# Kernel optimization log

Hardware: AMD Instinct MI355X
Metric: run time of the kernel (lower is better)

The kernel has to match this reference:

```python
import jax, jax.numpy as jnp
import numpy as np


def setup_inputs() -> dict:
    key = jax.random.key(0)
    ks = jax.random.split(key, 16)
    B, S, D = 2, 2048, 1024
    H, SH, RH = 16, 1, 3
    hd = D // H
    w = 1.0 / np.sqrt(D)
    return {
        "x": jax.random.normal(ks[0], (B, S, D), jnp.float32),
        "Wq": jax.random.normal(ks[1], (D, D), jnp.float32) * w,
        "bq": jnp.zeros((D,), jnp.float32),
        "Wk": jax.random.normal(ks[2], (D, D), jnp.float32) * w,
        "bk": jnp.zeros((D,), jnp.float32),
        "Wv": jax.random.normal(ks[3], (D, D), jnp.float32) * w,
        "bv": jnp.zeros((D,), jnp.float32),
        "Wproj": jax.random.normal(ks[4], (D, D), jnp.float32) * w,
        "bproj": jnp.zeros((D,), jnp.float32),
        "Wr": jax.random.normal(ks[5], (D, H - SH), jnp.float32) * w,
        "br": jnp.zeros((H - SH,), jnp.float32),
        "Ws": jax.random.normal(ks[6], (D, 2), jnp.float32) * w,
        "bs": jnp.zeros((2,), jnp.float32),
        "temperature": jnp.zeros((H, 1, 1), jnp.float32),
        "query_embedding": jax.random.truncated_normal(ks[7], -2.0, 2.0, (H, 1, hd), jnp.float32) * 0.02,
        "num_heads": H,
        "shared_heads": SH,
        "routed_heads": RH,
    }


def reference(x, Wq, bq, Wk, bk, Wv, bv, Wproj, bproj, Wr, br, Ws, bs,
              temperature, query_embedding, num_heads, shared_heads, routed_heads):
    B, S, D = x.shape
    H = num_heads
    hd = D // H

    def split_heads(t):  # [B,S,D] -> [B,H,S,hd]
        return t.reshape(B, S, H, hd).transpose(0, 2, 1, 3)

    q = split_heads(x @ Wq + bq)
    k = split_heads(x @ Wk + bk)
    v = split_heads(x @ Wv + bv)

    # L2-normalize q along head_dim, add learned query embedding, scale by softplus(temperature)
    q_norm = q * jax.lax.rsqrt(jnp.sum(q * q, axis=-1, keepdims=True) + 1e-12)
    q_scaled = (q_norm + query_embedding[None]) * jax.nn.softplus(temperature)[None]

    attn = jnp.einsum('bhqd,bhkd->bhqk', q_scaled, k) / jnp.sqrt(jnp.float32(hd))
    attn = jax.nn.softmax(attn, axis=-1)
    o = jnp.einsum('bhqk,bhkd->bhqd', attn, v)
    o = o.transpose(0, 2, 1, 3).reshape(B, S, D)  # [B,S,D]

    # Routed-head gating via top-k router
    gates = jax.nn.softmax(o @ Wr + br, axis=-1)          # [B,S,H-SH]
    _, idx = jax.lax.top_k(gates, routed_heads)           # [B,S,RH]
    mask = jax.nn.one_hot(idx, H - shared_heads, dtype=gates.dtype).sum(axis=2)
    routed_gates = gates * mask * jnp.float32(routed_heads)

    # Shared-head gating
    sw = jax.nn.softmax(o @ Ws + bs, axis=-1)             # [B,S,2]
    shared_gates = sw * jnp.float32(shared_heads)
    w0 = sw * 2.0
    shared_gates = w0[..., 0:1] * shared_gates
    routed_gates = w0[..., 1:2] * routed_gates
    masked_gates = jnp.concatenate([shared_gates, routed_gates], axis=-1)

    # einsum('bnh,bnd->bnd') sums over h: scales o by sum of gates
    o = masked_gates.sum(axis=-1, keepdims=True) * o
    return o @ Wproj + bproj
```

## Files before the change

### kernel.cpp

```cpp
#include <hip/hip_runtime.h>
#include <hip/hip_bf16.h>

typedef unsigned short ushort_t;
typedef unsigned int uint_t;

typedef __attribute__((ext_vector_type(8))) short bf8;
typedef __attribute__((ext_vector_type(4))) float f4;
typedef __attribute__((ext_vector_type(16))) float f16v;

__device__ __forceinline__ float bf2f(ushort_t u) {
    unsigned int x = ((unsigned int)u) << 16;
    return __uint_as_float(x);
}
__device__ __forceinline__ ushort_t f2bf(float f) {
    unsigned int x = __float_as_uint(f);
    unsigned int r = x + 0x7fffu + ((x >> 16) & 1u);
    return (ushort_t)(r >> 16);
}
__device__ __forceinline__ uint_t pack2bf(float a, float b) {
    return (uint_t)f2bf(a) | ((uint_t)f2bf(b) << 16);
}
__device__ __forceinline__ uint_t pack2bf_fast(float a, float b) {
    uint_t au = __float_as_uint(a) + 0x8000u;
    uint_t bu = __float_as_uint(b) + 0x8000u;
    return __builtin_amdgcn_perm(bu, au, 0x07060302);
}
__device__ __forceinline__ float exp2_fast(float x) {
    float r; asm("v_exp_f32 %0, %1" : "=v"(r) : "v"(x)); return r;
}
__device__ __forceinline__ uint_t cvtpk_bf16(float lo, float hi) {
    uint_t r; asm("v_cvt_pk_bf16_f32 %0, %1, %2" : "=v"(r) : "v"(lo), "v"(hi)); return r;
}
__device__ __forceinline__ void pl32swap(uint_t &a, uint_t &b) {
    asm("v_permlane32_swap_b32 %0, %1" : "+v"(a), "+v"(b));
}

__device__ __forceinline__ void gl2lds16(const ushort_t* g, ushort_t* l) {
    __builtin_amdgcn_global_load_lds(
        (const __attribute__((address_space(1))) void*)g,
        (__attribute__((address_space(3))) void*)l, 16, 0, 0);
}

__device__ __forceinline__ void waitl0() {
    asm volatile("s_waitcnt lgkmcnt(0)" ::: "memory");
    __builtin_amdgcn_sched_barrier(0);
}

__global__ __launch_bounds__(256)
void prep(const float* __restrict__ x, ushort_t* __restrict__ xb,
          const float* __restrict__ Wr, const float* __restrict__ Ws,
          ushort_t* __restrict__ Wg,
          const float* __restrict__ W0, const float* __restrict__ W1,
          const float* __restrict__ W2, const float* __restrict__ W3,
          ushort_t* __restrict__ T0, ushort_t* __restrict__ T1,
          ushort_t* __restrict__ T2, ushort_t* __restrict__ T3)
{
    __shared__ float tile[32][33];
    int bid = blockIdx.x;
    int t = threadIdx.x;
    if (bid < 4096) {
        int i = bid * 256 + t;
        float4 v = ((const float4*)x)[i];
        uint2 o;
        o.x = pack2bf(v.x, v.y);
        o.y = pack2bf(v.z, v.w);
        ((uint2*)xb)[i] = o;
    } else if (bid < 4224) {
        int idx = (bid - 4096) * 256 + t;
        int c = idx >> 10, d = idx & 1023;
        float v = 0.f;
        if (c < 15) v = Wr[(size_t)d * 15 + c];
        else if (c < 17) v = Ws[(size_t)d * 2 + (c - 15)];
        Wg[idx] = f2bf(v);
    } else {
        int idx = bid - 4224;
        int z = idx >> 10, r10 = idx & 1023;
        int k0 = (r10 & 31) * 32, n0 = (r10 >> 5) * 32;
        const float* W; ushort_t* T;
        switch (z) {
            case 0: W = W0; T = T0; break;
            case 1: W = W1; T = T1; break;
            case 2: W = W2; T = T2; break;
            default: W = W3; T = T3; break;
        }
        int r = t >> 3, c4 = (t & 7) * 4;
        float4 v = *(const float4*)&W[(size_t)(k0 + r) * 1024 + n0 + c4];
        tile[r][c4 + 0] = v.x; tile[r][c4 + 1] = v.y;
        tile[r][c4 + 2] = v.z; tile[r][c4 + 3] = v.w;
        __syncthreads();
        int n = t >> 3, kk = (t & 7) * 4;
        uint2 o;
        o.x = pack2bf(tile[kk][n], tile[kk + 1][n]);
        o.y = pack2bf(tile[kk + 2][n], tile[kk + 3][n]);
        *(uint2*)&T[(size_t)(n0 + n) * 1024 + k0 + kk] = o;
    }
}

__global__ __launch_bounds__(256)
void gemmQKV(const ushort_t* __restrict__ A, const ushort_t* __restrict__ Wt3,
             const float* __restrict__ bq, const float* __restrict__ bk,
             const float* __restrict__ bv,
             ushort_t* __restrict__ Qb, ushort_t* __restrict__ Kw,
             ushort_t* __restrict__ VTw,
             const float* __restrict__ temp, const float* __restrict__ emb)
{
    const int K = 1024;
    __shared__ ushort_t As[128 * 64];
    __shared__ ushort_t Bs[64 * 64];

    int t = threadIdx.x;
    int m0 = blockIdx.x * 128;
    int y = blockIdx.y;
    int region = y >> 4;
    int n0r = (y & 15) * 64;
    int head = y & 15;

    int lane = t & 63, w = t >> 6;
    int lm = lane & 15, quad = lane >> 4;
    int wm = w * 32;

    f4 acc[8] = {};

    int srow = t >> 3;
    int schunk = ((t & 7) ^ (srow & 7)) * 8;
    const ushort_t* pA = &A[(size_t)(m0 + srow) * K + schunk];
    const ushort_t* pB = &Wt3[(size_t)(y * 64 + srow) * K + schunk];
    const size_t rstep = (size_t)32 * K;

    for (int k0 = 0; k0 < K; k0 += 64) {
        #pragma unroll
        for (int j = 0; j < 4; j++)
            gl2lds16(pA + j * rstep, &As[(t + j * 256) * 8]);
        #pragma unroll
        for (int j = 0; j < 2; j++)
            gl2lds16(pB + j * rstep, &Bs[(t + j * 256) * 8]);
        pA += 64; pB += 64;
        __syncthreads();

        #pragma unroll
        for (int ks = 0; ks < 2; ks++) {
            int rc = ((ks * 4 + quad) ^ (lm & 7)) * 8;
            bf8 af[2], bfr[4];
            #pragma unroll
            for (int mi = 0; mi < 2; mi++)
                af[mi] = *(bf8*)&As[(wm + mi * 16 + lm) * 64 + rc];
            #pragma unroll
            for (int ni = 0; ni < 4; ni++)
                bfr[ni] = *(bf8*)&Bs[(ni * 16 + lm) * 64 + rc];
            if (region == 2) {
                #pragma unroll
                for (int mi = 0; mi < 2; mi++)
                #pragma unroll
                for (int ni = 0; ni < 4; ni++)
                    acc[mi * 4 + ni] = __builtin_amdgcn_mfma_f32_16x16x32_bf16(af[mi], bfr[ni], acc[mi * 4 + ni], 0, 0, 0);
            } else {
                #pragma unroll
                for (int ni = 0; ni < 4; ni++)
                #pragma unroll
                for (int mi = 0; mi < 2; mi++)
                    acc[ni * 2 + mi] = __builtin_amdgcn_mfma_f32_16x16x32_bf16(bfr[ni], af[mi], acc[ni * 2 + mi], 0, 0, 0);
            }
        }
        __syncthreads();
    }

    if (region == 0) {
        float sp = log1pf(__expf(temp[head]));
        float qs = sp * 0.18033688011112042f;
        f4 bv4[4], ev4[4];
        #pragma unroll
        for (int ni = 0; ni < 4; ni++) {
            bv4[ni] = *(const f4*)&bq[n0r + ni * 16 + quad * 4];
            ev4[ni] = *(const f4*)&emb[head * 64 + ni * 16 + quad * 4];
        }
        #pragma unroll
        for (int mi = 0; mi < 2; mi++) {
            float v[4][4];
            float ss = 0.f;
            #pragma unroll
            for (int ni = 0; ni < 4; ni++)
            #pragma unroll
            for (int i = 0; i < 4; i++) {
                v[ni][i] = acc[ni * 2 + mi][i] + bv4[ni][i];
                ss += v[ni][i] * v[ni][i];
            }
            ss += __shfl_xor(ss, 16, 64);
            ss += __shfl_xor(ss, 32, 64);
            float rs = rsqrtf(ss + 1e-12f);
            int tok = m0 + wm + mi * 16 + lm;
            int b = tok >> 11, s = tok & 2047;
            size_t rowb = (((size_t)(b * 16 + head)) * 2048 + s) * 64;
            #pragma unroll
            for (int ni = 0; ni < 4; ni++) {
                uint2 o;
                o.x = pack2bf((v[ni][0] * rs + ev4[ni][0]) * qs,
                              (v[ni][1] * rs + ev4[ni][1]) * qs);
                o.y = pack2bf((v[ni][2] * rs + ev4[ni][2]) * qs,
                              (v[ni][3] * rs + ev4[ni][3]) * qs);
                *(uint2*)&Qb[rowb + ni * 16 + quad * 4] = o;
            }
        }
    } else if (region == 1) {
        f4 bv4[4];
        #pragma unroll
        for (int ni = 0; ni < 4; ni++)
            bv4[ni] = *(const f4*)&bk[n0r + ni * 16 + quad * 4];
        #pragma unroll
        for (int mi = 0; mi < 2; mi++) {
            int tok = m0 + wm + mi * 16 + lm;
            int b = tok >> 11, s = tok & 2047;
            size_t rowb = (((size_t)(b * 16 + head)) * 2048 + s) * 64;
            #pragma unroll
            for (int ni = 0; ni < 4; ni++) {
                uint2 o;
                o.x = pack2bf(acc[ni * 2 + mi][0] + bv4[ni][0], acc[ni * 2 + mi][1] + bv4[ni][1]);
                o.y = pack2bf(acc[ni * 2 + mi][2] + bv4[ni][2], acc[ni * 2 + mi][3] + bv4[ni][3]);
                *(uint2*)&Kw[rowb + ni * 16 + quad * 4] = o;
            }
        }
    } else {
        float bvv[4];
        #pragma unroll
        for (int ni = 0; ni < 4; ni++) bvv[ni] = bv[n0r + ni * 16 + lm];
        #pragma unroll
        for (int mi = 0; mi < 2; mi++) {
            int gr0 = m0 + wm + mi * 16 + quad * 4;
            int b = gr0 >> 11, s0 = gr0 & 2047;
            #pragma unroll
            for (int ni = 0; ni < 4; ni++) {
                int d = ni * 16 + lm;
                uint2 o;
                o.x = pack2bf(acc[mi * 4 + ni][0] + bvv[ni], acc[mi * 4 + ni][1] + bvv[ni]);
                o.y = pack2bf(acc[mi * 4 + ni][2] + bvv[ni], acc[mi * 4 + ni][3] + bvv[ni]);
                *(uint2*)&VTw[(((size_t)(b * 16 + head)) * 64 + d) * 2048 + s0] = o;
            }
        }
    }
}

__global__ __launch_bounds__(256)
void gemmP(const ushort_t* __restrict__ A, const ushort_t* __restrict__ Wt,
           const float* __restrict__ bias, const float* __restrict__ G,
           float* __restrict__ out, int M, int N, int K)
{
    __shared__ ushort_t As[64 * 64];
    __shared__ ushort_t Bs[128 * 64];

    int t = threadIdx.x;
    int m0 = blockIdx.x * 64, n0 = blockIdx.y * 128;
    int lane = t & 63, w = t >> 6;
    int lm = lane & 15, quad = lane >> 4;
    int wm = (w >> 1) * 32, wn = (w & 1) * 64;

    f4 acc[4][2] = {};

    int srow = t >> 3;
    int schunk = ((t & 7) ^ (srow & 7)) * 8;
    const ushort_t* pA = &A[(size_t)(m0 + srow) * K + schunk];
    const ushort_t* pB = &Wt[(size_t)(n0 + srow) * K + schunk];
    const size_t rstep = (size_t)32 * K;

    for (int k0 = 0; k0 < K; k0 += 64) {
        gl2lds16(pA, &As[t * 8]);
        gl2lds16(pA + rstep, &As[(t + 256) * 8]);
        #pragma unroll
        for (int j = 0; j < 4; j++)
            gl2lds16(pB + j * rstep, &Bs[(t + j * 256) * 8]);
        pA += 64; pB += 64;
        __syncthreads();

        #pragma unroll
        for (int ks = 0; ks < 2; ks++) {
            int rc = ((ks * 4 + quad) ^ (lm & 7)) * 8;
            bf8 af[2], bfr[4];
            #pragma unroll
            for (int mi = 0; mi < 2; mi++)
                af[mi] = *(bf8*)&As[(wm + mi * 16 + lm) * 64 + rc];
            #pragma unroll
            for (int ni = 0; ni < 4; ni++)
                bfr[ni] = *(bf8*)&Bs[(wn + ni * 16 + lm) * 64 + rc];
            #pragma unroll
            for (int ni = 0; ni < 4; ni++)
            #pragma unroll
            for (int mi = 0; mi < 2; mi++)
                acc[ni][mi] = __builtin_amdgcn_mfma_f32_16x16x32_bf16(bfr[ni], af[mi], acc[ni][mi], 0, 0, 0);
        }
        __syncthreads();
    }

    f4 bv4[4];
    #pragma unroll
    for (int ni = 0; ni < 4; ni++)
        bv4[ni] = *(const f4*)&bias[n0 + wn + ni * 16 + quad * 4];
    #pragma unroll
    for (int mi = 0; mi < 2; mi++) {
        int tok = m0 + wm + mi * 16 + lm;
        float g = G[tok];
        size_t rowb = (size_t)tok * N + n0 + wn;
        #pragma unroll
        for (int ni = 0; ni < 4; ni++) {
            f4 o;
            #pragma unroll
            for (int i = 0; i < 4; i++) o[i] = g * acc[ni][mi][i] + bv4[ni][i];
            *(f4*)&out[rowb + ni * 16 + quad * 4] = o;
        }
    }
}

__global__ __launch_bounds__(256)
void attn(const ushort_t* __restrict__ Q, const ushort_t* __restrict__ K,
          const ushort_t* __restrict__ VT, ushort_t* __restrict__ Opart,
          float* __restrict__ Lw, int kps)
{
    __shared__ ushort_t Ks[64 * 72];
    __shared__ ushort_t Vt[64 * 72];

    int t = threadIdx.x, lane = t & 63, w = t >> 6;
    int l31 = lane & 31;
    uint_t hi = lane >> 5;
    int bid = blockIdx.x;
    int bh = bid & 31, qt = (bid >> 5) & 15, ks = bid >> 9;
    size_t base = (size_t)bh * 2048 * 64;

    int tok = qt * 128 + w * 32 + l31;
    const ushort_t* qp = &Q[base + (size_t)tok * 64 + hi * 8];
    bf8 qa[4];
    #pragma unroll
    for (int c = 0; c < 4; c++) qa[c] = *(const bf8*)(qp + c * 16);

    float l_part = 0.f;
    f16v o_acc[2] = {};

    int sr = t >> 3, sc = (t & 7) * 8;
    const ushort_t* kp = &K[base + (size_t)(ks * kps + sr) * 64 + sc];
    const ushort_t* vp = &VT[base + (size_t)sr * 2048 + ks * kps + sc];

    uint4 rk0 = *(const uint4*)(kp);
    uint4 rk1 = *(const uint4*)(kp + 32 * 64);
    uint4 rv0 = *(const uint4*)(vp);
    uint4 rv1 = *(const uint4*)(vp + 32 * 2048);
    kp += 64 * 64; vp += 64;

    int iters = kps >> 6;
    for (int it = 0; it < iters; ++it) {
        *(uint4*)&Ks[sr * 72 + sc] = rk0;
        *(uint4*)&Ks[(sr + 32) * 72 + sc] = rk1;
        *(uint4*)&Vt[sr * 72 + sc] = rv0;
        *(uint4*)&Vt[(sr + 32) * 72 + sc] = rv1;
        __syncthreads();

        rk0 = *(const uint4*)(kp);
        rk1 = *(const uint4*)(kp + 32 * 64);
        rv0 = *(const uint4*)(vp);
        rv1 = *(const uint4*)(vp + 32 * 2048);
        kp += 64 * 64; vp += 64;

        bf8 pf[4];
        #pragma unroll
        for (int kt2 = 0; kt2 < 2; kt2++) {
            f16v s = {};
            #pragma unroll
            for (int c = 0; c < 4; c++) {
                bf8 kf = *(bf8*)&Ks[(kt2 * 32 + l31) * 72 + c * 16 + hi * 8];
                s = __builtin_amdgcn_mfma_f32_32x32x16_bf16(kf, qa[c], s, 0, 0, 0);
            }
            uint_t px[4], py[4];
            #pragma unroll
            for (int g = 0; g < 4; g++) {
                float p0 = exp2_fast(s[g * 4 + 0]);
                float p1 = exp2_fast(s[g * 4 + 1]);
                float p2 = exp2_fast(s[g * 4 + 2]);
                float p3 = exp2_fast(s[g * 4 + 3]);
                l_part += (p0 + p1) + (p2 + p3);
                px[g] = cvtpk_bf16(p0, p1);
                py[g] = cvtpk_bf16(p2, p3);
            }
            #pragma unroll
            for (int cc = 0; cc < 2; cc++) {
                uint_t ax = px[2 * cc], bx = px[2 * cc + 1];
                uint_t ay = py[2 * cc], by = py[2 * cc + 1];
                pl32swap(ax, bx);
                pl32swap(ay, by);
                uint4 u;
                u.x = ax; u.y = ay; u.z = bx; u.w = by;
                pf[kt2 * 2 + cc] = *(bf8*)&u;
            }
        }

        #pragma unroll
        for (int c = 0; c < 4; c++) {
            #pragma unroll
            for (int dt = 0; dt < 2; dt++) {
                bf8 vf = *(bf8*)&Vt[(dt * 32 + l31) * 72 + c * 16 + hi * 8];
                o_acc[dt] = __builtin_amdgcn_mfma_f32_32x32x16_bf16(vf, pf[c], o_acc[dt], 0, 0, 0);
            }
        }
        __syncthreads();
    }

    l_part += __shfl_xor(l_part, 32, 64);
    if (hi == 0) Lw[((size_t)ks * 32 + bh) * 2048 + tok] = l_part;

    size_t pbase = (((size_t)(ks * 32 + bh)) * 2048 + tok) * 64;
    #pragma unroll
    for (int dt = 0; dt < 2; dt++)
    #pragma unroll
    for (int g = 0; g < 4; g++) {
        int d0 = dt * 32 + g * 8 + hi * 4;
        uint2 o;
        o.x = pack2bf_fast(o_acc[dt][g * 4 + 0], o_acc[dt][g * 4 + 1]);
        o.y = pack2bf_fast(o_acc[dt][g * 4 + 2], o_acc[dt][g * 4 + 3]);
        *(uint2*)&Opart[pbase + d0] = o;
    }
}

__global__ __launch_bounds__(256)
void fuseCR(const ushort_t* __restrict__ Opart, const float* __restrict__ Lw,
            const ushort_t* __restrict__ Wg, const float* __restrict__ br,
            const float* __restrict__ bs, ushort_t* __restrict__ Ob,
            float* __restrict__ G, int splits)
{
    __shared__ ushort_t Obs[16 * 1032];
    __shared__ float rl_s[16][16];
    __shared__ float Ls[16][21];

    int t = threadIdx.x;
    int tokg0 = blockIdx.x * 16;
    int b = tokg0 >> 11, st0 = tokg0 & 2047;

    {
        int h = t >> 4, tt = t & 15;
        size_t row = (size_t)(b * 16 + h) * 2048 + st0 + tt;
        float l = 0.f;
        #pragma unroll 4
        for (int s = 0; s < splits; s++) l += Lw[(size_t)s * 65536 + row];
        rl_s[h][tt] = 1.f / l;
    }
    __syncthreads();

    {
        int tt = t >> 4, dc = (t & 15) * 4;
        #pragma unroll 4
        for (int h = 0; h < 16; h++) {
            size_t rbase = ((size_t)(b * 16 + h) * 2048 + st0 + tt) * 64 + dc;
            float v0 = 0.f, v1 = 0.f, v2 = 0.f, v3 = 0.f;
            #pragma unroll 4
            for (int s = 0; s < splits; s++) {
                uint2 p = *(const uint2*)&Opart[(size_t)s * 4194304 + rbase];
                v0 += bf2f(p.x & 0xffff);
                v1 += bf2f(p.x >> 16);
                v2 += bf2f(p.y & 0xffff);
                v3 += bf2f(p.y >> 16);
            }
            float rl = rl_s[h][tt];
            v0 *= rl; v1 *= rl; v2 *= rl; v3 *= rl;
            uint2 o;
            o.x = pack2bf(v0, v1);
            o.y = pack2bf(v2, v3);
            *(uint2*)&Obs[tt * 1032 + h * 64 + dc] = o;
            *(uint2*)&Ob[((size_t)(tokg0 + tt)) * 1024 + h * 64 + dc] = o;
        }
    }
    __syncthreads();

    if (t < 64) {
        int lm = t & 15, quad = t >> 4;
        const ushort_t* b0p = &Wg[(size_t)lm * 1024 + quad * 8];
        const ushort_t* b1p = &Wg[(size_t)(16 + lm) * 1024 + quad * 8];
        f4 acc0 = {}, acc1 = {};
        for (int k0 = 0; k0 < 1024; k0 += 32) {
            bf8 a  = *(const bf8*)&Obs[lm * 1032 + k0 + quad * 8];
            bf8 b0 = *(const bf8*)(b0p + k0);
            bf8 b1 = *(const bf8*)(b1p + k0);
            acc0 = __builtin_amdgcn_mfma_f32_16x16x32_bf16(a, b0, acc0, 0, 0, 0);
            acc1 = __builtin_amdgcn_mfma_f32_16x16x32_bf16(a, b1, acc1, 0, 0, 0);
        }
        #pragma unroll
        for (int i = 0; i < 4; i++) {
            int tl = quad * 4 + i;
            Ls[tl][lm] = acc0[i];
            if (lm == 0) Ls[tl][16] = acc1[i];
        }
        waitl0();

        if (t < 16) {
            float v[15];
            float mx = -1e30f;
            #pragma unroll
            for (int c = 0; c < 15; c++) { v[c] = Ls[t][c] + br[c]; mx = fmaxf(mx, v[c]); }
            float sum = 0.f;
            #pragma unroll
            for (int c = 0; c < 15; c++) { v[c] = __expf(v[c] - mx); sum += v[c]; }
            float inv = 1.f / sum;
            float t3 = 0.f;
            for (int r = 0; r < 3; r++) {
                int bi = 0; float bv = -1e30f;
                #pragma unroll
                for (int c = 0; c < 15; c++) if (v[c] > bv) { bv = v[c]; bi = c; }
                t3 += bv; v[bi] = -1e30f;
            }
            t3 *= inv;
            float a0 = Ls[t][15] + bs[0], a1 = Ls[t][16] + bs[1];
            float m2 = fmaxf(a0, a1);
            float e0 = __expf(a0 - m2), e1 = __expf(a1 - m2);
            G[tokg0 + t] = (2.f * e0 + 6.f * e1 * t3) / (e0 + e1);
        }
    }
}

extern "C" void kernel_launch(void* const* d_in, const int* in_sizes, int n_in,
                              void* d_out, int out_size, void* d_ws, size_t ws_size,
                              hipStream_t stream)
{
    const float* x     = (const float*)d_in[0];
    const float* Wq    = (const float*)d_in[1];
    const float* bq    = (const float*)d_in[2];
    const float* Wk    = (const float*)d_in[3];
    const float* bk    = (const float*)d_in[4];
    const float* Wv    = (const float*)d_in[5];
    const float* bv    = (const float*)d_in[6];
    const float* Wproj = (const float*)d_in[7];
    const float* bproj = (const float*)d_in[8];
    const float* Wr    = (const float*)d_in[9];
    const float* br    = (const float*)d_in[10];
    const float* Ws    = (const float*)d_in[11];
    const float* bs    = (const float*)d_in[12];
    const float* temp  = (const float*)d_in[13];
    const float* emb   = (const float*)d_in[14];

    const int M = 4096, N = 1024, Kd = 1024;

    char* ws = (char*)d_ws;
    ushort_t* Kw    = (ushort_t*)ws;
    ushort_t* VTw   = (ushort_t*)(ws + 8388608);
    ushort_t* Qb    = (ushort_t*)(ws + 16777216);
    ushort_t* Wtp   = (ushort_t*)(ws + 25165824);
    float*    Gw    = (float*)(ws + 27262976);
    ushort_t* Wg    = (ushort_t*)(ws + 27279360);
    ushort_t* Wt3   = (ushort_t*)(ws + 27869184);
    ushort_t* Opart = (ushort_t*)(ws + 27869184);
    ushort_t* xb    = (ushort_t*)(ws + 34160640);
    ushort_t* Ob    = Qb;

    int SK;
    float* Lw;
    if (ws_size >= 62472192) {
        SK = 4;
        Lw = (float*)(ws + 61423616);
    } else {
        SK = 2;
        Lw = (float*)(ws + 27344896);
    }

    prep<<<8320, 256, 0, stream>>>(x, xb, Wr, Ws, Wg, Wq, Wk, Wv, Wproj,
        Wt3, Wt3 + 1048576, Wt3 + 2097152, Wtp);

    gemmQKV<<<dim3(32, 48), 256, 0, stream>>>(xb, Wt3, bq, bk, bv,
        Qb, Kw, VTw, temp, emb);

    attn<<<512 * SK, 256, 0, stream>>>(Qb, Kw, VTw, Opart, Lw, 2048 / SK);

    fuseCR<<<256, 256, 0, stream>>>(Opart, Lw, Wg, br, bs, Ob, Gw, SK);

    gemmP<<<dim3(64, 8), 256, 0, stream>>>(Ob, Wtp, bproj, Gw, (float*)d_out, M, N, Kd);
}
```

Before: 237.0 us.

## Double-buffer K/V shared tiles in attention and fix split-K to two

Measured after the change: 235.1 us. About the same (-0.8%).

```diff
diff --git a/kernel.cpp b/kernel.cpp
--- a/kernel.cpp
+++ b/kernel.cpp
@@ -312,8 +312,8 @@
           const ushort_t* __restrict__ VT, ushort_t* __restrict__ Opart,
           float* __restrict__ Lw, int kps)
 {
-    __shared__ ushort_t Ks[64 * 72];
-    __shared__ ushort_t Vt[64 * 72];
+    __shared__ ushort_t Ks[2][64 * 72];
+    __shared__ ushort_t Vt[2][64 * 72];
 
     int t = threadIdx.x, lane = t & 63, w = t >> 6;
     int l31 = lane & 31;
@@ -340,28 +340,44 @@
     uint4 rv0 = *(const uint4*)(vp);
     uint4 rv1 = *(const uint4*)(vp + 32 * 2048);
     kp += 64 * 64; vp += 64;
-
+    *(uint4*)&Ks[0][sr * 72 + sc] = rk0;
+    *(uint4*)&Ks[0][(sr + 32) * 72 + sc] = rk1;
+    *(uint4*)&Vt[0][sr * 72 + sc] = rv0;
+    *(uint4*)&Vt[0][(sr + 32) * 72 + sc] = rv1;
+    rk0 = *(const uint4*)(kp);
+    rk1 = *(const uint4*)(kp + 32 * 64);
+    rv0 = *(const uint4*)(vp);
+    rv1 = *(const uint4*)(vp + 32 * 2048);
+    kp += 64 * 64; vp += 64;
+    __syncthreads();
+
+    int cur = 0;
     int iters = kps >> 6;
     for (int it = 0; it < iters; ++it) {
-        *(uint4*)&Ks[sr * 72 + sc] = rk0;
-        *(uint4*)&Ks[(sr + 32) * 72 + sc] = rk1;
-        *(uint4*)&Vt[sr * 72 + sc] = rv0;
-        *(uint4*)&Vt[(sr + 32) * 72 + sc] = rv1;
-        __syncthreads();
-
+        {
+            ushort_t* Kw_ = &Ks[cur ^ 1][0];
+            ushort_t* Vw_ = &Vt[cur ^ 1][0];
+            *(uint4*)&Kw_[sr * 72 + sc] = rk0;
+            *(uint4*)&Kw_[(sr + 32) * 72 + sc] = rk1;
+            *(uint4*)&Vw_[sr * 72 + sc] = rv0;
+            *(uint4*)&Vw_[(sr + 32) * 72 + sc] = rv1;
+        }
         rk0 = *(const uint4*)(kp);
         rk1 = *(const uint4*)(kp + 32 * 64);
         rv0 = *(const uint4*)(vp);
         rv1 = *(const uint4*)(vp + 32 * 2048);
         kp += 64 * 64; vp += 64;
 
+        const ushort_t* Kr = &Ks[cur][0];
+        const ushort_t* Vr = &Vt[cur][0];
+
         bf8 pf[4];
         #pragma unroll
         for (int kt2 = 0; kt2 < 2; kt2++) {
             f16v s = {};
             #pragma unroll
             for (int c = 0; c < 4; c++) {
-                bf8 kf = *(bf8*)&Ks[(kt2 * 32 + l31) * 72 + c * 16 + hi * 8];
+                bf8 kf = *(bf8*)&Kr[(kt2 * 32 + l31) * 72 + c * 16 + hi * 8];
                 s = __builtin_amdgcn_mfma_f32_32x32x16_bf16(kf, qa[c], s, 0, 0, 0);
             }
             uint_t px[4], py[4];
@@ -391,11 +407,12 @@
         for (int c = 0; c < 4; c++) {
             #pragma unroll
             for (int dt = 0; dt < 2; dt++) {
-                bf8 vf = *(bf8*)&Vt[(dt * 32 + l31) * 72 + c * 16 + hi * 8];
+                bf8 vf = *(bf8*)&Vr[(dt * 32 + l31) * 72 + c * 16 + hi * 8];
                 o_acc[dt] = __builtin_amdgcn_mfma_f32_32x32x16_bf16(vf, pf[c], o_acc[dt], 0, 0, 0);
             }
         }
         __syncthreads();
+        cur ^= 1;
     }
 
     l_part += __shfl_xor(l_part, 32, 64);
@@ -537,20 +554,13 @@
     ushort_t* Wtp   = (ushort_t*)(ws + 25165824);
     float*    Gw    = (float*)(ws + 27262976);
     ushort_t* Wg    = (ushort_t*)(ws + 27279360);
+    float*    Lw    = (float*)(ws + 27344896);
     ushort_t* Wt3   = (ushort_t*)(ws + 27869184);
     ushort_t* Opart = (ushort_t*)(ws + 27869184);
     ushort_t* xb    = (ushort_t*)(ws + 34160640);
     ushort_t* Ob    = Qb;
 
-    int SK;
-    float* Lw;
-    if (ws_size >= 62472192) {
-        SK = 4;
-        Lw = (float*)(ws + 61423616);
-    } else {
-        SK = 2;
-        Lw = (float*)(ws + 27344896);
-    }
+    const int SK = 2;
 
     prep<<<8320, 256, 0, stream>>>(x, xb, Wr, Ws, Wg, Wq, Wk, Wv, Wproj,
         Wt3, Wt3 + 1048576, Wt3 + 2097152, Wtp);
```
